# Performance work log

Hardware: AMD Instinct MI355X
Metric: run time of the kernel (lower is better)

## Reference

```python
import jax, jax.numpy as jnp
import numpy as np

B, S, D = 4, 2048, 512
H, DQK, DV = 6, 64, 64
PROJ = (DQK + DQK + DV) * H  # 1152
EPS = 1e-5


def setup_inputs() -> dict:
    key = jax.random.key(0)
    ks = jax.random.split(key, 5)
    sc = 0.05
    return {
        "x": jax.random.normal(ks[0], (B, S, D), jnp.float32),
        "Wp": jax.random.normal(ks[1], (PROJ, D), jnp.float32) * sc,
        "bp": jax.random.normal(ks[2], (PROJ,), jnp.float32) * sc,
        "Wo": jax.random.normal(ks[3], (D, H * DV), jnp.float32) * sc,
        "bo": jax.random.normal(ks[4], (D,), jnp.float32) * sc,
        "gamma": jnp.ones((D,), jnp.float32),
        "beta": jnp.zeros((D,), jnp.float32),
    }


def reference(x, Wp, bp, Wo, bo, gamma, beta):
    b, s, d = x.shape
    # 1x1 Conv1d projection == pointwise linear: [b,s,d] @ [d,proj] -> [b,s,proj]
    proj = jnp.einsum("bsd,pd->bsp", x, Wp) + bp
    q, k, v = proj[..., : H * DQK], proj[..., H * DQK : 2 * H * DQK], proj[..., 2 * H * DQK :]
    # split heads -> [b,h,s,depth]
    q = q.reshape(b, s, H, DQK).transpose(0, 2, 1, 3)
    k = k.reshape(b, s, H, DQK).transpose(0, 2, 1, 3)
    v = v.reshape(b, s, H, DV).transpose(0, 2, 1, 3)
    scores = jnp.einsum("bhqd,bhkd->bhqk", q, k) / jnp.sqrt(jnp.float32(DQK))
    attn = jax.nn.softmax(scores, axis=-1)  # softmax over kv axis
    out = jnp.einsum("bhqk,bhkd->bhqd", attn, v)
    # concat heads -> [b,s,h*dv]
    concat = out.transpose(0, 2, 1, 3).reshape(b, s, H * DV)
    y = jnp.einsum("bsf,df->bsd", concat, Wo) + bo
    z = x + y
    mu = jnp.mean(z, axis=-1, keepdims=True)
    var = jnp.mean(jnp.square(z - mu), axis=-1, keepdims=True)
    return (z - mu) / jnp.sqrt(var + EPS) * gamma + beta
```

## Files before the change

### kernel.cpp

```cpp
#include <hip/hip_runtime.h>

typedef __bf16 bf16;
typedef __bf16 bf16x8 __attribute__((ext_vector_type(8)));
typedef __bf16 bf16x4 __attribute__((ext_vector_type(4)));
typedef float  f32x4  __attribute__((ext_vector_type(4)));

#define BB 4
#define SS 2048
#define DD 512
#define HH 6
#define DH 64
#define PROJ 1152
#define FF 384
#define LDK 72
#define NSPLIT 4

__device__ __forceinline__ bool probe_fp32(const unsigned* p) {
    return p[0] == 0x3F800000u;
}

__device__ __forceinline__ float fast_exp2(float x) {
#if __has_builtin(__builtin_amdgcn_exp2f)
    return __builtin_amdgcn_exp2f(x);
#else
    return __expf(x * 0.69314718f);
#endif
}

struct CvtSrcs { const void* s[7]; };

#define CB0 524288
#define CB1 598016
#define CB2 622592
#define CB3 622736
#define CB4 622800
#define CB5 622864
#define CB6 622928

__global__ __launch_bounds__(256) void cvt_all_kernel(
    CvtSrcs srcs, bf16* __restrict__ dst, const unsigned* __restrict__ probe)
{
    const int t = blockIdx.x * 256 + threadIdx.x;
    if (t >= CB6) return;
    int seg, base;
    if      (t < CB0) { seg = 0; base = 0;   }
    else if (t < CB1) { seg = 1; base = CB0; }
    else if (t < CB2) { seg = 2; base = CB1; }
    else if (t < CB3) { seg = 3; base = CB2; }
    else if (t < CB4) { seg = 4; base = CB3; }
    else if (t < CB5) { seg = 5; base = CB4; }
    else              { seg = 6; base = CB5; }
    const int li = (t - base) * 8;
    if (probe_fp32(probe)) {
        const float* s = (const float*)srcs.s[seg] + li;
        bf16x8 o;
#pragma unroll
        for (int j = 0; j < 8; ++j) o[j] = (bf16)s[j];
        *(bf16x8*)&dst[(size_t)t * 8] = o;
    } else {
        *(bf16x8*)&dst[(size_t)t * 8] =
            *(const bf16x8*)((const bf16*)srcs.s[seg] + li);
    }
}

template<int MERGE>
__global__ __launch_bounds__(256) void gemm_bt_kernel(
    const bf16* __restrict__ A, const float* __restrict__ lpart,
    const bf16* __restrict__ B, const bf16* __restrict__ bias,
    bf16* __restrict__ Cout, int M, int N, int K)
{
    __shared__ __attribute__((aligned(16))) bf16 sA[64 * LDK];
    __shared__ __attribute__((aligned(16))) bf16 sB[128 * LDK];

    const int tid  = threadIdx.x;
    const int lane = tid & 63;
    const int wave = tid >> 6;
    const int wn = wave * 32;
    const int l15 = lane & 15;
    const int quad = lane >> 4;
    const int bm = blockIdx.x * 64;
    const int bn = blockIdx.y * 128;
    const int KT = K / 64;

    const size_t PS = (size_t)BB * HH * SS * DH;
    const size_t LS = (size_t)BB * HH * SS;

    int srowA[2], srowB[4];
    const int scol = (tid & 7) << 3;
#pragma unroll
    for (int j = 0; j < 2; ++j) srowA[j] = (j * 256 + tid) >> 3;
#pragma unroll
    for (int j = 0; j < 4; ++j) srowB[j] = (j * 256 + tid) >> 3;

    const bf16* pA[2]; const bf16* pB[4];
    const float* pl0[2];
#pragma unroll
    for (int j = 0; j < 2; ++j) {
        if (MERGE) {
            int row = bm + srowA[j];
            int b = row >> 11, q = row & (SS - 1);
            pA[j]  = A + ((size_t)(b * HH) * SS + q) * DH + scol;
            pl0[j] = lpart + (size_t)(b * HH) * SS + q;
        } else {
            pA[j] = A + (size_t)(bm + srowA[j]) * K + scol;
        }
    }
#pragma unroll
    for (int j = 0; j < 4; ++j)
        pB[j] = B + (size_t)(bn + srowB[j]) * K + scol;

    bf16x8 arb[2], brb[4];
    bf16x8 arm[2][NSPLIT];
    float  lm[2][NSPLIT];

    auto loadAB = [&]() {
#pragma unroll
        for (int j = 0; j < 2; ++j) {
            if (MERGE) {
#pragma unroll
                for (int p = 0; p < NSPLIT; ++p) {
                    arm[j][p] = *(const bf16x8*)(pA[j] + (size_t)p * PS);
                    lm[j][p]  = pl0[j][(size_t)p * LS];
                }
                pA[j]  += (size_t)SS * DH;
                pl0[j] += SS;
            } else {
                arb[j] = *(const bf16x8*)pA[j];
                pA[j] += 64;
            }
        }
#pragma unroll
        for (int j = 0; j < 4; ++j) {
            brb[j] = *(const bf16x8*)pB[j];
            pB[j] += 64;
        }
    };

    loadAB();

    const f32x4 fzero = {0.f, 0.f, 0.f, 0.f};
    f32x4 acc[4][2];
#pragma unroll
    for (int mi = 0; mi < 4; ++mi)
#pragma unroll
        for (int ni = 0; ni < 2; ++ni) acc[mi][ni] = fzero;

    for (int kt = 0; kt < KT; ++kt) {
        __syncthreads();
#pragma unroll
        for (int j = 0; j < 2; ++j) {
            if (MERGE) {
                float lsum = 0.f;
#pragma unroll
                for (int p = 0; p < NSPLIT; ++p) lsum += lm[j][p];
                float inv = 1.f / lsum;
                bf16x8 m;
#pragma unroll
                for (int e = 0; e < 8; ++e) {
                    float s = 0.f;
#pragma unroll
                    for (int p = 0; p < NSPLIT; ++p) s += (float)arm[j][p][e];
                    m[e] = (bf16)(s * inv);
                }
                *(bf16x8*)&sA[srowA[j] * LDK + scol] = m;
            } else {
                *(bf16x8*)&sA[srowA[j] * LDK + scol] = arb[j];
            }
        }
#pragma unroll
        for (int j = 0; j < 4; ++j)
            *(bf16x8*)&sB[srowB[j] * LDK + scol] = brb[j];
        __syncthreads();
        if (kt + 1 < KT) loadAB();

#pragma unroll
        for (int kk = 0; kk < 2; ++kk) {
            bf16x8 af[4], bfr[2];
#pragma unroll
            for (int i = 0; i < 4; ++i)
                af[i] = *(const bf16x8*)&sA[(i * 16 + l15) * LDK + kk * 32 + quad * 8];
#pragma unroll
            for (int i = 0; i < 2; ++i)
                bfr[i] = *(const bf16x8*)&sB[(wn + i * 16 + l15) * LDK + kk * 32 + quad * 8];
#pragma unroll
            for (int mi = 0; mi < 4; ++mi)
#pragma unroll
                for (int ni = 0; ni < 2; ++ni)
                    acc[mi][ni] = __builtin_amdgcn_mfma_f32_16x16x32_bf16(
                        af[mi], bfr[ni], acc[mi][ni], 0, 0, 0);
        }
    }

#pragma unroll
    for (int mi = 0; mi < 4; ++mi) {
        int row = bm + mi * 16 + quad * 4;
#pragma unroll
        for (int ni = 0; ni < 2; ++ni) {
            int col = bn + wn + ni * 16 + l15;
            float bv = (float)bias[col];
#pragma unroll
            for (int r = 0; r < 4; ++r)
                Cout[(size_t)(row + r) * N + col] = (bf16)(acc[mi][ni][r] + bv);
        }
    }
}

__global__ __launch_bounds__(256) void vt_kernel(
    const bf16* __restrict__ proj, bf16* __restrict__ Vt)
{
    __shared__ __attribute__((aligned(16))) bf16 lt[64 * LDK];

    const int tid = threadIdx.x;
    const int s0 = blockIdx.x * 64;
    const int bh = blockIdx.y;
    const int b = bh / HH, h = bh % HH;

#pragma unroll
    for (int i = 0; i < 2; ++i) {
        int vid = i * 256 + tid;
        int sl = vid >> 3;
        int dc = (vid & 7) << 3;
        bf16x8 v = *(const bf16x8*)&proj[
            (size_t)(b * SS + s0 + sl) * PROJ + 2 * HH * DH + h * DH + dc];
#pragma unroll
        for (int j = 0; j < 8; ++j) {
            int d = dc + j;
            lt[d * LDK + (sl ^ (((d >> 3) & 3) * 8))] = v[j];
        }
    }
    __syncthreads();

#pragma unroll
    for (int i = 0; i < 2; ++i) {
        int vid = i * 256 + tid;
        int d = vid >> 3;
        int sc = (vid & 7) << 3;
        bf16x8 v = *(const bf16x8*)&lt[d * LDK + (sc ^ (((d >> 3) & 3) * 8))];
        *(bf16x8*)&Vt[(size_t)bh * DH * SS + (size_t)d * SS + s0 + sc] = v;
    }
}

__global__ __launch_bounds__(256) void attn_kernel(
    const bf16* __restrict__ proj, const bf16* __restrict__ Vt,
    bf16* __restrict__ Opart, float* __restrict__ lpart)
{
    __shared__ __attribute__((aligned(16))) bf16 sK [64 * 64];
    __shared__ __attribute__((aligned(16))) bf16 sVt[64 * 64];
    __shared__ __attribute__((aligned(16))) bf16 sP [4 * 32 * 64];

    const int tid  = threadIdx.x;
    const int lane = tid & 63;
    const int wave = tid >> 6;
    const int l15  = lane & 15;
    const int quad = lane >> 4;

    const int bh = blockIdx.y;
    const int b = bh / HH, h = bh % HH;
    const int q0 = blockIdx.x * 128;
    const int kz = blockIdx.z;
    const bf16* base = proj + (size_t)b * SS * PROJ;
    const bf16* vtb  = Vt + (size_t)bh * DH * SS;

    const int sr = tid >> 3;
    const int sc = (tid & 7) << 3;

    const float QS = 0.18033688f;
    bf16x8 qf[2][2];
#pragma unroll
    for (int g = 0; g < 2; ++g) {
        const int qrow = q0 + wave * 32 + g * 16 + l15;
#pragma unroll
        for (int ks = 0; ks < 2; ++ks) {
            qf[ks][g] = *(const bf16x8*)&base[
                (size_t)qrow * PROJ + h * DH + ks * 32 + quad * 8];
#pragma unroll
            for (int j = 0; j < 8; ++j)
                qf[ks][g][j] = (bf16)((float)qf[ks][g][j] * QS);
        }
    }

    const f32x4 fzero = {0.f, 0.f, 0.f, 0.f};
    f32x4 lacc[2] = {fzero, fzero};
    f32x4 oacc[2][4];
#pragma unroll
    for (int g = 0; g < 2; ++g)
#pragma unroll
        for (int fi = 0; fi < 4; ++fi) oacc[g][fi] = fzero;

    bf16* pw = &sP[wave * 32 * 64];

    const int TILES = SS / (64 * NSPLIT);
    const int kt0 = kz * TILES;
    const int kt1 = kt0 + TILES;

    const bf16* pk[2]; const bf16* pv[2];
#pragma unroll
    for (int i = 0; i < 2; ++i) {
        int r = i * 32 + sr;
        pk[i] = &base[(size_t)(kt0 * 64 + r) * PROJ + HH * DH + h * DH + sc];
        pv[i] = &vtb[(size_t)r * SS + kt0 * 64 + sc];
    }
    auto loadKV = [&](bf16x8 (&kr)[2], bf16x8 (&vr)[2]) {
#pragma unroll
        for (int i = 0; i < 2; ++i) {
            kr[i] = *(const bf16x8*)pk[i];
            vr[i] = *(const bf16x8*)pv[i];
            pk[i] += (size_t)64 * PROJ;
            pv[i] += 64;
        }
    };

    bf16x8 kA[2], vA[2], kB[2], vB[2];
    loadKV(kA, vA);
    loadKV(kB, vB);

    auto tile = [&](int kt, bf16x8 (&kr)[2], bf16x8 (&vr)[2]) {
        __syncthreads();
#pragma unroll
        for (int i = 0; i < 2; ++i) {
            int r = i * 32 + sr;
            const int swc = sc ^ ((r & 7) << 3);
            *(bf16x8*)&sK [r * 64 + swc] = kr[i];
            *(bf16x8*)&sVt[r * 64 + swc] = vr[i];
        }
        __syncthreads();
        if (kt + 2 < kt1) loadKV(kr, vr);

        f32x4 st[2][4];
#pragma unroll
        for (int mi = 0; mi < 4; ++mi) {
            const int row = mi * 16 + l15;
            const int sw = (row & 7) << 3;
            bf16x8 af0 = *(const bf16x8*)&sK[row * 64 + ((quad * 8) ^ sw)];
            bf16x8 af1 = *(const bf16x8*)&sK[row * 64 + ((32 + quad * 8) ^ sw)];
#pragma unroll
            for (int g = 0; g < 2; ++g) {
                st[g][mi] = __builtin_amdgcn_mfma_f32_16x16x32_bf16(
                    af0, qf[0][g], fzero, 0, 0, 0);
                st[g][mi] = __builtin_amdgcn_mfma_f32_16x16x32_bf16(
                    af1, qf[1][g], st[g][mi], 0, 0, 0);
            }
        }

#pragma unroll
        for (int g = 0; g < 2; ++g)
#pragma unroll
            for (int mi = 0; mi < 4; ++mi) {
#pragma unroll
                for (int r = 0; r < 4; ++r)
                    st[g][mi][r] = fast_exp2(st[g][mi][r]);
                lacc[g] += st[g][mi];
            }

#pragma unroll
        for (int g = 0; g < 2; ++g) {
            const int r = g * 16 + l15;
            const int sw = (r & 7) << 3;
#pragma unroll
            for (int mi = 0; mi < 4; ++mi) {
                bf16x4 p4;
#pragma unroll
                for (int e = 0; e < 4; ++e) p4[e] = (bf16)st[g][mi][e];
                *(bf16x4*)&pw[r * 64 + ((mi * 16 + quad * 4) ^ sw)] = p4;
            }
        }

#pragma unroll
        for (int ks = 0; ks < 2; ++ks) {
            bf16x8 bfrag[2];
#pragma unroll
            for (int g = 0; g < 2; ++g) {
                const int r = g * 16 + l15;
                bfrag[g] = *(const bf16x8*)&pw[
                    r * 64 + ((ks * 32 + quad * 8) ^ ((r & 7) << 3))];
            }
#pragma unroll
            for (int fi = 0; fi < 4; ++fi) {
                const int row = fi * 16 + l15;
                bf16x8 af = *(const bf16x8*)&sVt[
                    row * 64 + ((ks * 32 + quad * 8) ^ ((row & 7) << 3))];
#pragma unroll
                for (int g = 0; g < 2; ++g)
                    oacc[g][fi] = __builtin_amdgcn_mfma_f32_16x16x32_bf16(
                        af, bfrag[g], oacc[g][fi], 0, 0, 0);
            }
        }
    };

    for (int kt = kt0; kt < kt1; kt += 2) {
        tile(kt,     kA, vA);
        tile(kt + 1, kB, vB);
    }

    float l_part[2];
#pragma unroll
    for (int g = 0; g < 2; ++g) {
        l_part[g] = lacc[g][0] + lacc[g][1] + lacc[g][2] + lacc[g][3];
        l_part[g] += __shfl_xor(l_part[g], 16);
        l_part[g] += __shfl_xor(l_part[g], 32);
    }

    const size_t zoff = (size_t)(kz * BB * HH + bh) * SS;
#pragma unroll
    for (int g = 0; g < 2; ++g) {
        const int qg = q0 + wave * 32 + g * 16 + l15;
        bf16* orow = Opart + (zoff + qg) * DH;
#pragma unroll
        for (int fi = 0; fi < 4; ++fi) {
            bf16x4 o4;
#pragma unroll
            for (int r = 0; r < 4; ++r) o4[r] = (bf16)oacc[g][fi][r];
            *(bf16x4*)&orow[fi * 16 + quad * 4] = o4;
        }
    }
    if (lane < 16) {
#pragma unroll
        for (int g = 0; g < 2; ++g)
            lpart[zoff + q0 + wave * 32 + g * 16 + lane] = l_part[g];
    }
}

__global__ __launch_bounds__(256) void ln_kernel(
    const bf16* __restrict__ x, const bf16* __restrict__ y,
    const bf16* __restrict__ gamma, const bf16* __restrict__ beta,
    void* __restrict__ out, const unsigned* __restrict__ probe)
{
    const bool f32 = probe_fp32(probe);
    const int lane = threadIdx.x & 63;
    const int wave = threadIdx.x >> 6;
    const int row = blockIdx.x * 4 + wave;
    const size_t off = (size_t)row * DD + lane * 8;

    bf16x8 xv = *(const bf16x8*)&x[off];
    bf16x8 yv = *(const bf16x8*)&y[off];
    float z[8];
    float s = 0.f;
#pragma unroll
    for (int j = 0; j < 8; ++j) { z[j] = (float)xv[j] + (float)yv[j]; s += z[j]; }
#pragma unroll
    for (int m = 1; m < 64; m <<= 1) s += __shfl_xor(s, m);
    float mu = s * (1.f / DD);
    float s2 = 0.f;
#pragma unroll
    for (int j = 0; j < 8; ++j) { float d = z[j] - mu; s2 += d * d; }
#pragma unroll
    for (int m = 1; m < 64; m <<= 1) s2 += __shfl_xor(s2, m);
    float rs = rsqrtf(s2 * (1.f / DD) + 1e-5f);

    bf16x8 gm = *(const bf16x8*)&gamma[lane * 8];
    bf16x8 be = *(const bf16x8*)&beta[lane * 8];
    if (f32) {
        f32x4 o0, o1;
#pragma unroll
        for (int j = 0; j < 4; ++j) {
            o0[j] = (z[j]     - mu) * rs * (float)gm[j]     + (float)be[j];
            o1[j] = (z[j + 4] - mu) * rs * (float)gm[j + 4] + (float)be[j + 4];
        }
        *(f32x4*)&((float*)out)[off]     = o0;
        *(f32x4*)&((float*)out)[off + 4] = o1;
    } else {
        bf16x8 o;
#pragma unroll
        for (int j = 0; j < 8; ++j)
            o[j] = (bf16)((z[j] - mu) * rs * (float)gm[j] + (float)be[j]);
        *(bf16x8*)&((bf16*)out)[off] = o;
    }
}

extern "C" void kernel_launch(void* const* d_in, const int* in_sizes, int n_in,
                              void* d_out, int out_size, void* d_ws, size_t ws_size,
                              hipStream_t stream)
{
    const unsigned* probe = (const unsigned*)d_in[5];

    char* ws = (char*)d_ws;
    size_t o = 0;
    bf16* xb   = (bf16*)(ws + o); o += (size_t)BB * SS * DD * 2;
    bf16* Wpb  = (bf16*)(ws + o); o += (size_t)PROJ * DD * 2;
    bf16* Wob  = (bf16*)(ws + o); o += (size_t)DD * FF * 2;
    bf16* bpb  = (bf16*)(ws + o); o += PROJ * 2;
    bf16* bob  = (bf16*)(ws + o); o += DD * 2;
    bf16* gb   = (bf16*)(ws + o); o += DD * 2;
    bf16* bb   = (bf16*)(ws + o); o += DD * 2;
    bf16* proj   = (bf16*)(ws + o); o += (size_t)BB * SS * PROJ * 2;
    bf16* vtbuf  = (bf16*)(ws + o); o += (size_t)BB * HH * DH * SS * 2;
    bf16* Opart  = (bf16*)(ws + o); o += (size_t)NSPLIT * BB * HH * SS * DH * 2;
    float* lpart = (float*)(ws + o); o += (size_t)NSPLIT * BB * HH * SS * 4;
    bf16* ybuf = proj;

    CvtSrcs srcs;
    srcs.s[0] = d_in[0]; srcs.s[1] = d_in[1]; srcs.s[2] = d_in[3];
    srcs.s[3] = d_in[2]; srcs.s[4] = d_in[4]; srcs.s[5] = d_in[5];
    srcs.s[6] = d_in[6];
    cvt_all_kernel<<<(CB6 + 255) / 256, 256, 0, stream>>>(srcs, xb, probe);

    gemm_bt_kernel<0><<<dim3((BB * SS) / 64, PROJ / 128), 256, 0, stream>>>(
        xb, nullptr, Wpb, bpb, proj, BB * SS, PROJ, DD);
    vt_kernel<<<dim3(SS / 64, BB * HH), 256, 0, stream>>>(proj, vtbuf);
    attn_kernel<<<dim3(SS / 128, BB * HH, NSPLIT), 256, 0, stream>>>(
        proj, vtbuf, Opart, lpart);
    gemm_bt_kernel<1><<<dim3((BB * SS) / 64, DD / 128), 256, 0, stream>>>(
        Opart, lpart, Wob, bob, ybuf, BB * SS, DD, FF);
    ln_kernel<<<dim3((BB * SS) / 4), 256, 0, stream>>>(
        xb, ybuf, gb, bb, d_out, probe);
}
```

Measured before the change: 162.8 us.

## Rewrite attention with 32x32 MFMA, register-resident P via permlane swap, double-buffered LDS

The attention inner loop moves from 16x16x32 to 32x32x16 bf16 MFMA tiles. The P matrix stays in registers: it is packed with v_cvt_pk_bf16 and rearranged with permlane32_swap into the B-fragment layout, which removes the LDS round trip for P. K/V tiles are double-buffered in LDS so there is one barrier per tile, and the KV split count drops from 4 to 2. The aim is to cut LDS traffic and barriers and use larger MFMAs, at the cost of fewer blocks and less parallelism from the smaller split, plus reliance on gfx950-specific instructions.

```diff
diff --git a/kernel.cpp b/kernel.cpp
--- a/kernel.cpp
+++ b/kernel.cpp
@@ -4,6 +4,9 @@
 typedef __bf16 bf16x8 __attribute__((ext_vector_type(8)));
 typedef __bf16 bf16x4 __attribute__((ext_vector_type(4)));
 typedef float  f32x4  __attribute__((ext_vector_type(4)));
+typedef float  f32x16 __attribute__((ext_vector_type(16)));
+typedef unsigned uint2v __attribute__((ext_vector_type(2)));
+typedef unsigned uint4v __attribute__((ext_vector_type(4)));
 
 #define BB 4
 #define SS 2048
@@ -13,7 +16,7 @@
 #define PROJ 1152
 #define FF 384
 #define LDK 72
-#define NSPLIT 4
+#define NSPLIT 2
 
 __device__ __forceinline__ bool probe_fp32(const unsigned* p) {
     return p[0] == 0x3F800000u;
@@ -24,6 +27,21 @@
     return __builtin_amdgcn_exp2f(x);
 #else
     return __expf(x * 0.69314718f);
+#endif
+}
+
+__device__ __forceinline__ unsigned cvt_pk_bf16(float lo, float hi) {
+    unsigned r;
+    asm("v_cvt_pk_bf16_f32 %0, %1, %2" : "=v"(r) : "v"(lo), "v"(hi));
+    return r;
+}
+
+__device__ __forceinline__ void plswap(unsigned &a, unsigned &b) {
+#if __has_builtin(__builtin_amdgcn_permlane32_swap)
+    uint2v r = __builtin_amdgcn_permlane32_swap(a, b, false, false);
+    a = r[0]; b = r[1];
+#else
+    asm volatile("v_permlane32_swap_b32 %0, %1" : "+v"(a), "+v"(b));
 #endif
 }
 
@@ -244,15 +262,14 @@
     const bf16* __restrict__ proj, const bf16* __restrict__ Vt,
     bf16* __restrict__ Opart, float* __restrict__ lpart)
 {
-    __shared__ __attribute__((aligned(16))) bf16 sK [64 * 64];
-    __shared__ __attribute__((aligned(16))) bf16 sVt[64 * 64];
-    __shared__ __attribute__((aligned(16))) bf16 sP [4 * 32 * 64];
+    __shared__ __attribute__((aligned(16))) bf16 sK [2][64 * 64];
+    __shared__ __attribute__((aligned(16))) bf16 sVt[2][64 * 64];
 
     const int tid  = threadIdx.x;
     const int lane = tid & 63;
     const int wave = tid >> 6;
-    const int l15  = lane & 15;
-    const int quad = lane >> 4;
+    const int l31  = lane & 31;
+    const int hi   = lane >> 5;
 
     const int bh = blockIdx.y;
     const int b = bh / HH, h = bh % HH;
@@ -265,29 +282,23 @@
     const int sc = (tid & 7) << 3;
 
     const float QS = 0.18033688f;
-    bf16x8 qf[2][2];
-#pragma unroll
-    for (int g = 0; g < 2; ++g) {
-        const int qrow = q0 + wave * 32 + g * 16 + l15;
-#pragma unroll
-        for (int ks = 0; ks < 2; ++ks) {
-            qf[ks][g] = *(const bf16x8*)&base[
-                (size_t)qrow * PROJ + h * DH + ks * 32 + quad * 8];
-#pragma unroll
-            for (int j = 0; j < 8; ++j)
-                qf[ks][g][j] = (bf16)((float)qf[ks][g][j] * QS);
-        }
-    }
-
-    const f32x4 fzero = {0.f, 0.f, 0.f, 0.f};
-    f32x4 lacc[2] = {fzero, fzero};
-    f32x4 oacc[2][4];
-#pragma unroll
-    for (int g = 0; g < 2; ++g)
-#pragma unroll
-        for (int fi = 0; fi < 4; ++fi) oacc[g][fi] = fzero;
-
-    bf16* pw = &sP[wave * 32 * 64];
+    const int qrow = q0 + wave * 32 + l31;
+    bf16x8 qf[4];
+#pragma unroll
+    for (int s = 0; s < 4; ++s) {
+        qf[s] = *(const bf16x8*)&base[
+            (size_t)qrow * PROJ + h * DH + s * 16 + hi * 8];
+#pragma unroll
+        for (int j = 0; j < 8; ++j)
+            qf[s][j] = (bf16)((float)qf[s][j] * QS);
+    }
+
+    f32x16 oacc[2];
+#pragma unroll
+    for (int df = 0; df < 2; ++df)
+#pragma unroll
+        for (int r = 0; r < 16; ++r) oacc[df][r] = 0.f;
+    float lsum = 0.f;
 
     const int TILES = SS / (64 * NSPLIT);
     const int kt0 = kz * TILES;
@@ -300,7 +311,9 @@
         pk[i] = &base[(size_t)(kt0 * 64 + r) * PROJ + HH * DH + h * DH + sc];
         pv[i] = &vtb[(size_t)r * SS + kt0 * 64 + sc];
     }
-    auto loadKV = [&](bf16x8 (&kr)[2], bf16x8 (&vr)[2]) {
+
+    bf16x8 kr[2], vr[2];
+    auto loadKV = [&]() {
 #pragma unroll
         for (int i = 0; i < 2; ++i) {
             kr[i] = *(const bf16x8*)pk[i];
@@ -309,115 +322,99 @@
             pv[i] += 64;
         }
     };
-
-    bf16x8 kA[2], vA[2], kB[2], vB[2];
-    loadKV(kA, vA);
-    loadKV(kB, vB);
-
-    auto tile = [&](int kt, bf16x8 (&kr)[2], bf16x8 (&vr)[2]) {
-        __syncthreads();
+    auto stage = [&](int buf) {
 #pragma unroll
         for (int i = 0; i < 2; ++i) {
             int r = i * 32 + sr;
             const int swc = sc ^ ((r & 7) << 3);
-            *(bf16x8*)&sK [r * 64 + swc] = kr[i];
-            *(bf16x8*)&sVt[r * 64 + swc] = vr[i];
-        }
+            *(bf16x8*)&sK [buf][r * 64 + swc] = kr[i];
+            *(bf16x8*)&sVt[buf][r * 64 + swc] = vr[i];
+        }
+    };
+
+    loadKV();
+    stage(0);
+    loadKV();
+
+    const f32x16 fz16 = {0.f,0.f,0.f,0.f,0.f,0.f,0.f,0.f,
+                         0.f,0.f,0.f,0.f,0.f,0.f,0.f,0.f};
+
+    for (int t = kt0; t < kt1; ++t) {
+        const int cur = t & 1;
         __syncthreads();
-        if (kt + 2 < kt1) loadKV(kr, vr);
-
-        f32x4 st[2][4];
-#pragma unroll
-        for (int mi = 0; mi < 4; ++mi) {
-            const int row = mi * 16 + l15;
+        if (t + 1 < kt1) {
+            stage(cur ^ 1);
+            if (t + 2 < kt1) loadKV();
+        }
+
+        f32x16 st[2];
+#pragma unroll
+        for (int it = 0; it < 2; ++it) {
+            const int row = it * 32 + l31;
             const int sw = (row & 7) << 3;
-            bf16x8 af0 = *(const bf16x8*)&sK[row * 64 + ((quad * 8) ^ sw)];
-            bf16x8 af1 = *(const bf16x8*)&sK[row * 64 + ((32 + quad * 8) ^ sw)];
-#pragma unroll
-            for (int g = 0; g < 2; ++g) {
-                st[g][mi] = __builtin_amdgcn_mfma_f32_16x16x32_bf16(
-                    af0, qf[0][g], fzero, 0, 0, 0);
-                st[g][mi] = __builtin_amdgcn_mfma_f32_16x16x32_bf16(
-                    af1, qf[1][g], st[g][mi], 0, 0, 0);
+            st[it] = fz16;
+#pragma unroll
+            for (int s = 0; s < 4; ++s) {
+                bf16x8 kf = *(const bf16x8*)&sK[cur][
+                    row * 64 + ((s * 16 + hi * 8) ^ sw)];
+                st[it] = __builtin_amdgcn_mfma_f32_32x32x16_bf16(
+                    kf, qf[s], st[it], 0, 0, 0);
             }
         }
 
 #pragma unroll
-        for (int g = 0; g < 2; ++g)
-#pragma unroll
-            for (int mi = 0; mi < 4; ++mi) {
-#pragma unroll
-                for (int r = 0; r < 4; ++r)
-                    st[g][mi][r] = fast_exp2(st[g][mi][r]);
-                lacc[g] += st[g][mi];
+        for (int it = 0; it < 2; ++it)
+#pragma unroll
+            for (int r = 0; r < 16; ++r) {
+                st[it][r] = fast_exp2(st[it][r]);
+                lsum += st[it][r];
             }
 
-#pragma unroll
-        for (int g = 0; g < 2; ++g) {
-            const int r = g * 16 + l15;
-            const int sw = (r & 7) << 3;
-#pragma unroll
-            for (int mi = 0; mi < 4; ++mi) {
-                bf16x4 p4;
-#pragma unroll
-                for (int e = 0; e < 4; ++e) p4[e] = (bf16)st[g][mi][e];
-                *(bf16x4*)&pw[r * 64 + ((mi * 16 + quad * 4) ^ sw)] = p4;
+        unsigned pkt[2][4][2];
+#pragma unroll
+        for (int it = 0; it < 2; ++it)
+#pragma unroll
+            for (int j = 0; j < 4; ++j) {
+                pkt[it][j][0] = cvt_pk_bf16(st[it][4*j+0], st[it][4*j+1]);
+                pkt[it][j][1] = cvt_pk_bf16(st[it][4*j+2], st[it][4*j+3]);
             }
-        }
-
-#pragma unroll
-        for (int ks = 0; ks < 2; ++ks) {
-            bf16x8 bfrag[2];
-#pragma unroll
-            for (int g = 0; g < 2; ++g) {
-                const int r = g * 16 + l15;
-                bfrag[g] = *(const bf16x8*)&pw[
-                    r * 64 + ((ks * 32 + quad * 8) ^ ((r & 7) << 3))];
+
+#pragma unroll
+        for (int ks = 0; ks < 4; ++ks) {
+            const int it = ks >> 1, j0 = (ks & 1) * 2;
+            unsigned a0 = pkt[it][j0][0], b0 = pkt[it][j0 + 1][0];
+            unsigned a1 = pkt[it][j0][1], b1 = pkt[it][j0 + 1][1];
+            plswap(a0, b0);
+            plswap(a1, b1);
+            uint4v u = {a0, a1, b0, b1};
+            bf16x8 pfrag = __builtin_bit_cast(bf16x8, u);
+#pragma unroll
+            for (int df = 0; df < 2; ++df) {
+                const int row = df * 32 + l31;
+                const int sw = (row & 7) << 3;
+                bf16x8 vf = *(const bf16x8*)&sVt[cur][
+                    row * 64 + ((ks * 16 + hi * 8) ^ sw)];
+                oacc[df] = __builtin_amdgcn_mfma_f32_32x32x16_bf16(
+                    vf, pfrag, oacc[df], 0, 0, 0);
             }
-#pragma unroll
-            for (int fi = 0; fi < 4; ++fi) {
-                const int row = fi * 16 + l15;
-                bf16x8 af = *(const bf16x8*)&sVt[
-                    row * 64 + ((ks * 32 + quad * 8) ^ ((row & 7) << 3))];
-#pragma unroll
-                for (int g = 0; g < 2; ++g)
-                    oacc[g][fi] = __builtin_amdgcn_mfma_f32_16x16x32_bf16(
-                        af, bfrag[g], oacc[g][fi], 0, 0, 0);
-            }
-        }
-    };
-
-    for (int kt = kt0; kt < kt1; kt += 2) {
-        tile(kt,     kA, vA);
-        tile(kt + 1, kB, vB);
-    }
-
-    float l_part[2];
-#pragma unroll
-    for (int g = 0; g < 2; ++g) {
-        l_part[g] = lacc[g][0] + lacc[g][1] + lacc[g][2] + lacc[g][3];
-        l_part[g] += __shfl_xor(l_part[g], 16);
-        l_part[g] += __shfl_xor(l_part[g], 32);
-    }
+        }
+    }
+
+    lsum += __shfl_xor(lsum, 32);
 
     const size_t zoff = (size_t)(kz * BB * HH + bh) * SS;
-#pragma unroll
-    for (int g = 0; g < 2; ++g) {
-        const int qg = q0 + wave * 32 + g * 16 + l15;
-        bf16* orow = Opart + (zoff + qg) * DH;
-#pragma unroll
-        for (int fi = 0; fi < 4; ++fi) {
+    bf16* orow = Opart + (zoff + qrow) * DH;
+#pragma unroll
+    for (int df = 0; df < 2; ++df)
+#pragma unroll
+        for (int j = 0; j < 4; ++j) {
             bf16x4 o4;
 #pragma unroll
-            for (int r = 0; r < 4; ++r) o4[r] = (bf16)oacc[g][fi][r];
-            *(bf16x4*)&orow[fi * 16 + quad * 4] = o4;
-        }
-    }
-    if (lane < 16) {
-#pragma unroll
-        for (int g = 0; g < 2; ++g)
-            lpart[zoff + q0 + wave * 32 + g * 16 + lane] = l_part[g];
-    }
+            for (int r = 0; r < 4; ++r) o4[r] = (bf16)oacc[df][4*j + r];
+            *(bf16x4*)&orow[df * 32 + 8 * j + 4 * hi] = o4;
+        }
+    if (lane < 32)
+        lpart[zoff + q0 + wave * 32 + l31] = lsum;
 }
 
 __global__ __launch_bounds__(256) void ln_kernel(
```

Measured after the change: 161.7 us. No clear change (-0.7%).
